# Performance work log

Measured on AMD Instinct MI355X. Metric: run time of the kernel, lower is better.

The kernel has to match this reference:

```python
import jax, jax.numpy as jnp
import numpy as np

BN_EPS = 1e-5

def setup_inputs() -> dict:
    key = jax.random.key(0)
    k1, k2, k3 = jax.random.split(key, 3)
    B, N, K, C, Cout = 8, 16384, 16, 128, 256
    x = jax.random.normal(k1, (B, N, C), dtype=jnp.float32)
    edge_index = jax.random.randint(k2, (B, N, K), 0, N, dtype=jnp.int64)
    W = jax.random.normal(k3, (Cout, 2 * C), dtype=jnp.float32) * (1.0 / np.sqrt(2 * C))
    b = jnp.zeros((Cout,), dtype=jnp.float32)
    gamma = jnp.ones((Cout,), dtype=jnp.float32)
    beta = jnp.zeros((Cout,), dtype=jnp.float32)
    return {"x": x, "edge_index": edge_index, "W": W, "b": b, "gamma": gamma, "beta": beta}

def reference(x, edge_index, W, b, gamma, beta):
    B, N, C = x.shape
    # gather neighbors: [B, N, K, C]
    neighbors = x[jnp.arange(B)[:, None, None], edge_index]
    # max-relative aggregation: max_j x_j - x_i
    agg = neighbors.max(axis=2) - x                      # [B, N, C]
    h = jnp.concatenate([x, agg], axis=-1).reshape(B * N, 2 * C)
    y = h @ W.T + b                                      # Linear -> [B*N, Cout]
    # BatchNorm1d (training mode: batch statistics, biased variance)
    mean = y.mean(axis=0)
    var = y.var(axis=0)
    y = (y - mean) * jax.lax.rsqrt(var + BN_EPS) * gamma + beta
    out = jax.nn.gelu(y, approximate=False)
    return out.reshape(B, N, -1)
```

## Files before the change

### kernel.cpp

```cpp
#include <hip/hip_runtime.h>
#include <math.h>

constexpr int B_ = 8;
constexpr int N_ = 16384;
constexpr int C_ = 128;
constexpr int K_ = 16;
constexpr int CO = 256;
constexpr int TC = 256;
constexpr int M_ = B_ * N_;
constexpr int TM = 64;
constexpr int NB = M_ / TM;
constexpr int NCHUNK = 8;

typedef _Float16 h8 __attribute__((ext_vector_type(8)));
typedef float f4 __attribute__((ext_vector_type(4)));

__device__ __forceinline__ float4 f4max(float4 a, float4 b) {
  return make_float4(fmaxf(a.x, b.x), fmaxf(a.y, b.y),
                     fmaxf(a.z, b.z), fmaxf(a.w, b.w));
}

__device__ __forceinline__ ushort4 pack_h4(float4 v) {
  union { _Float16 h[4]; ushort4 u; } cv;
  cv.h[0] = (_Float16)v.x; cv.h[1] = (_Float16)v.y;
  cv.h[2] = (_Float16)v.z; cv.h[3] = (_Float16)v.w;
  return cv.u;
}

__global__ void k0_prep(const float* __restrict__ W, _Float16* __restrict__ Wf) {
  int g = blockIdx.x * 256 + threadIdx.x;
  int cout = g >> 5;
  int G = g & 31;
  int kk = G >> 2, go = G & 3;
  int nt = cout >> 4, c15 = cout & 15;
  const float* src = W + (size_t)cout * TC + G * 8;
  _Float16* dst = Wf + kk * 8192 + nt * 512 + (c15 + 16 * go) * 8;
  #pragma unroll
  for (int j = 0; j < 8; ++j) dst[j] = (_Float16)src[j];
}

__global__ __launch_bounds__(256, 3)
void k1_fused(const float* __restrict__ x, const int* __restrict__ eidx,
              const _Float16* __restrict__ Wf, const float* __restrict__ bias,
              float* __restrict__ y, double* __restrict__ stats)
{
  __shared__ __align__(16) _Float16 hsf[TM * TC];
  __shared__ __align__(16) int ids[TM * K_];

  const int tid = threadIdx.x;
  const int wave = tid >> 6;
  const int lane = tid & 63;
  const int batch = blockIdx.x & 7;
  const int tile = blockIdx.x >> 3;
  const long long row0 = (long long)batch * N_ + (long long)tile * TM;
  const float* __restrict__ xb = x + (size_t)batch * N_ * C_;

  ((int4*)ids)[tid] = ((const int4*)(eidx + row0 * K_))[tid];
  __syncthreads();

  #pragma unroll
  for (int it = 0; it < 8; ++it) {
    int w = it * 256 + tid;
    int m = w >> 5;
    int cq = (w & 31) << 2;
    float4 xv = *(const float4*)(x + (row0 + m) * (size_t)C_ + cq);
    float4 mx = make_float4(-INFINITY, -INFINITY, -INFINITY, -INFINITY);
    #pragma unroll
    for (int j = 0; j < K_; ++j) {
      int nb = ids[m * K_ + j];
      mx = f4max(mx, *(const float4*)(xb + (size_t)nb * C_ + cq));
    }
    int a0 = ((m >> 4) << 13) | ((cq >> 3) << 8) | ((m & 15) << 4) | ((cq & 4) << 1);
    a0 ^= ((a0 >> 8) & 7) << 4;
    *(ushort4*)((char*)hsf + a0) = pack_h4(xv);
    float4 dv = make_float4(mx.x - xv.x, mx.y - xv.y, mx.z - xv.z, mx.w - xv.w);
    int c2 = 128 + cq;
    int a1 = ((m >> 4) << 13) | ((c2 >> 3) << 8) | ((m & 15) << 4) | ((c2 & 4) << 1);
    a1 ^= ((a1 >> 8) & 7) << 4;
    *(ushort4*)((char*)hsf + a1) = pack_h4(dv);
  }
  __syncthreads();

  f4 acc[4][4] = {};
  #pragma unroll
  for (int kk = 0; kk < NCHUNK; ++kk) {
    h8 af[4], bf[4];
    #pragma unroll
    for (int nt = 0; nt < 4; ++nt)
      bf[nt] = *(const h8*)((const char*)Wf + (kk << 14) + (wave << 12) + (nt << 10) + (lane << 4));
    #pragma unroll
    for (int mt = 0; mt < 4; ++mt) {
      int off = (mt << 13) + (kk << 10) + lane * 16;
      off ^= ((off >> 8) & 7) << 4;
      af[mt] = *(const h8*)((const char*)hsf + off);
    }
    #pragma unroll
    for (int mt = 0; mt < 4; ++mt)
      #pragma unroll
      for (int nt = 0; nt < 4; ++nt)
        acc[mt][nt] = __builtin_amdgcn_mfma_f32_16x16x32_f16(af[mt], bf[nt], acc[mt][nt], 0, 0, 0);
  }

  const int c15 = lane & 15;
  const int rg = lane >> 4;
  float s4[4] = {0.f, 0.f, 0.f, 0.f};
  float q4[4] = {0.f, 0.f, 0.f, 0.f};
  #pragma unroll
  for (int nt = 0; nt < 4; ++nt) {
    int col = (wave << 6) + (nt << 4) + c15;
    float bb = bias[col];
    #pragma unroll
    for (int mt = 0; mt < 4; ++mt) {
      #pragma unroll
      for (int r = 0; r < 4; ++r) {
        float v = acc[mt][nt][r] + bb;
        long long row = row0 + (mt << 4) + (rg << 2) + r;
        y[row * CO + col] = v;
        s4[nt] += v;
        q4[nt] += v * v;
      }
    }
  }
  #pragma unroll
  for (int nt = 0; nt < 4; ++nt) {
    s4[nt] += __shfl_xor(s4[nt], 16, 64);
    s4[nt] += __shfl_xor(s4[nt], 32, 64);
    q4[nt] += __shfl_xor(q4[nt], 16, 64);
    q4[nt] += __shfl_xor(q4[nt], 32, 64);
  }
  if (lane < 16) {
    #pragma unroll
    for (int nt = 0; nt < 4; ++nt) {
      int col = (wave << 6) + (nt << 4) + c15;
      atomicAdd(&stats[col], (double)s4[nt]);
      atomicAdd(&stats[col + 256], (double)q4[nt]);
    }
  }
}

__global__ void k2_stats(const double* __restrict__ stats,
                         const float* __restrict__ gamma,
                         const float* __restrict__ beta,
                         float* __restrict__ ss) {
  int c = threadIdx.x;
  double mean = stats[c] * (1.0 / M_);
  double var  = stats[256 + c] * (1.0 / M_) - mean * mean;
  double scale = (double)gamma[c] / sqrt(var + 1e-5);
  ss[c]       = (float)scale;
  ss[256 + c] = (float)((double)beta[c] - mean * scale);
}

__global__ __launch_bounds__(256)
void k3_bn_gelu(float* __restrict__ y, const float* __restrict__ ss) {
  __shared__ float s_sc[CO], s_sh[CO];
  s_sc[threadIdx.x] = ss[threadIdx.x];
  s_sh[threadIdx.x] = ss[256 + threadIdx.x];
  __syncthreads();
  const float inv_sqrt2 = 0.70710678118654752440f;
  size_t i = (size_t)blockIdx.x * blockDim.x + threadIdx.x;
  const size_t stride = (size_t)gridDim.x * blockDim.x;
  const size_t total = (size_t)M_ * CO / 4;
  float4* y4 = (float4*)y;
  for (; i < total; i += stride) {
    float4 v = y4[i];
    int c4 = (int)(i & (CO / 4 - 1)) * 4;
    float4 r;
    { float u = v.x * s_sc[c4 + 0] + s_sh[c4 + 0]; r.x = 0.5f * u * (1.f + erff(u * inv_sqrt2)); }
    { float u = v.y * s_sc[c4 + 1] + s_sh[c4 + 1]; r.y = 0.5f * u * (1.f + erff(u * inv_sqrt2)); }
    { float u = v.z * s_sc[c4 + 2] + s_sh[c4 + 2]; r.z = 0.5f * u * (1.f + erff(u * inv_sqrt2)); }
    { float u = v.w * s_sc[c4 + 3] + s_sh[c4 + 3]; r.w = 0.5f * u * (1.f + erff(u * inv_sqrt2)); }
    y4[i] = r;
  }
}

extern "C" void kernel_launch(void* const* d_in, const int* in_sizes, int n_in,
                              void* d_out, int out_size, void* d_ws, size_t ws_size,
                              hipStream_t stream)
{
  const float* x     = (const float*)d_in[0];
  const int*   eidx  = (const int*)d_in[1];
  const float* W     = (const float*)d_in[2];
  const float* bias  = (const float*)d_in[3];
  const float* gamma = (const float*)d_in[4];
  const float* beta  = (const float*)d_in[5];
  float* y = (float*)d_out;
  char* ws = (char*)d_ws;

  _Float16* Wf    = (_Float16*)ws;
  double*   stats = (double*)(ws + 131072);
  float*    ss    = (float*)(ws + 131072 + 4096);

  hipMemsetAsync(stats, 0, 512 * sizeof(double), stream);
  k0_prep<<<32, 256, 0, stream>>>(W, Wf);
  k1_fused<<<NB, 256, 0, stream>>>(x, eidx, Wf, bias, y, stats);
  k2_stats<<<1, 256, 0, stream>>>(stats, gamma, beta, ss);
  k3_bn_gelu<<<2048, 256, 0, stream>>>(y, ss);
}
```

Measured before the change: 324.8 us.

## Gather neighbors from fp16 copy of x and use polynomial erf in GELU

Adds a pre-pass that converts x to fp16 in workspace, so the neighbor gather and max in the fused kernel read half the bytes and work on 8 channels per load. The fp32 path is kept as a fallback when the workspace is too small. The BN+GELU kernel replaces erff with an Abramowitz-Stegun polynomial approximation and loads scale/shift once per thread into registers instead of shared memory. Occupancy hint on the fused kernel rises from 3 to 4. This adds an extra conversion pass over x and some precision loss in the gather, max and GELU.

```diff
diff --git a/kernel.cpp b/kernel.cpp
--- a/kernel.cpp
+++ b/kernel.cpp
@@ -27,6 +27,32 @@
   return cv.u;
 }
 
+__device__ __forceinline__ uint4 hmax4(uint4 a, uint4 b) {
+  union U { uint4 u; _Float16 h[8]; } ua, ub, r;
+  ua.u = a; ub.u = b;
+  #pragma unroll
+  for (int i = 0; i < 8; ++i) r.h[i] = ua.h[i] > ub.h[i] ? ua.h[i] : ub.h[i];
+  return r.u;
+}
+
+__device__ __forceinline__ uint4 hsub4(uint4 a, uint4 b) {
+  union U { uint4 u; _Float16 h[8]; } ua, ub, r;
+  ua.u = a; ub.u = b;
+  #pragma unroll
+  for (int i = 0; i < 8; ++i) r.h[i] = ua.h[i] - ub.h[i];
+  return r.u;
+}
+
+__device__ __forceinline__ float gelu_f(float u) {
+  float z = fabsf(u) * 0.70710678118654752f;
+  float t = 1.0f / (1.0f + 0.3275911f * z);
+  float p = t * (0.254829592f + t * (-0.284496736f + t * (1.421413741f +
+            t * (-1.453152027f + t * 1.061405429f))));
+  float erfz = 1.0f - p * __expf(-z * z);
+  erfz = copysignf(erfz, u);
+  return 0.5f * u * (1.0f + erfz);
+}
+
 __global__ void k0_prep(const float* __restrict__ W, _Float16* __restrict__ Wf) {
   int g = blockIdx.x * 256 + threadIdx.x;
   int cout = g >> 5;
@@ -39,10 +65,22 @@
   for (int j = 0; j < 8; ++j) dst[j] = (_Float16)src[j];
 }
 
-__global__ __launch_bounds__(256, 3)
+__global__ __launch_bounds__(256)
+void k0b_cvt(const float* __restrict__ x, _Float16* __restrict__ xh) {
+  const size_t total = (size_t)M_ * C_ / 4;
+  const size_t stride = (size_t)gridDim.x * 256;
+  for (size_t i = (size_t)blockIdx.x * 256 + threadIdx.x; i < total; i += stride) {
+    float4 a = ((const float4*)x)[i];
+    ((ushort4*)xh)[i] = pack_h4(a);
+  }
+}
+
+template <int FP16>
+__global__ __launch_bounds__(256, 4)
 void k1_fused(const float* __restrict__ x, const int* __restrict__ eidx,
               const _Float16* __restrict__ Wf, const float* __restrict__ bias,
-              float* __restrict__ y, double* __restrict__ stats)
+              float* __restrict__ y, double* __restrict__ stats,
+              const _Float16* __restrict__ xh)
 {
   __shared__ __align__(16) _Float16 hsf[TM * TC];
   __shared__ __align__(16) int ids[TM * K_];
@@ -53,31 +91,56 @@
   const int batch = blockIdx.x & 7;
   const int tile = blockIdx.x >> 3;
   const long long row0 = (long long)batch * N_ + (long long)tile * TM;
-  const float* __restrict__ xb = x + (size_t)batch * N_ * C_;
 
   ((int4*)ids)[tid] = ((const int4*)(eidx + row0 * K_))[tid];
   __syncthreads();
 
-  #pragma unroll
-  for (int it = 0; it < 8; ++it) {
-    int w = it * 256 + tid;
-    int m = w >> 5;
-    int cq = (w & 31) << 2;
-    float4 xv = *(const float4*)(x + (row0 + m) * (size_t)C_ + cq);
-    float4 mx = make_float4(-INFINITY, -INFINITY, -INFINITY, -INFINITY);
-    #pragma unroll
-    for (int j = 0; j < K_; ++j) {
-      int nb = ids[m * K_ + j];
-      mx = f4max(mx, *(const float4*)(xb + (size_t)nb * C_ + cq));
-    }
-    int a0 = ((m >> 4) << 13) | ((cq >> 3) << 8) | ((m & 15) << 4) | ((cq & 4) << 1);
-    a0 ^= ((a0 >> 8) & 7) << 4;
-    *(ushort4*)((char*)hsf + a0) = pack_h4(xv);
-    float4 dv = make_float4(mx.x - xv.x, mx.y - xv.y, mx.z - xv.z, mx.w - xv.w);
-    int c2 = 128 + cq;
-    int a1 = ((m >> 4) << 13) | ((c2 >> 3) << 8) | ((m & 15) << 4) | ((c2 & 4) << 1);
-    a1 ^= ((a1 >> 8) & 7) << 4;
-    *(ushort4*)((char*)hsf + a1) = pack_h4(dv);
+  if constexpr (FP16) {
+    const _Float16* __restrict__ xbh = xh + (size_t)batch * N_ * C_;
+    #pragma unroll
+    for (int it = 0; it < 4; ++it) {
+      int w = it * 256 + tid;
+      int m = w >> 4;
+      int ch8 = (w & 15) << 3;
+      uint4 xv = *(const uint4*)(xh + (row0 + m) * (size_t)C_ + ch8);
+      uint4 mx = *(const uint4*)(xbh + (size_t)ids[m * K_] * C_ + ch8);
+      #pragma unroll
+      for (int j = 1; j < K_; ++j) {
+        int nb = ids[m * K_ + j];
+        mx = hmax4(mx, *(const uint4*)(xbh + (size_t)nb * C_ + ch8));
+      }
+      uint4 dv = hsub4(mx, xv);
+      int a0 = ((m >> 4) << 13) | ((ch8 >> 3) << 8) | ((m & 15) << 4);
+      a0 ^= ((a0 >> 8) & 7) << 4;
+      *(uint4*)((char*)hsf + a0) = xv;
+      int c2 = 128 + ch8;
+      int a1 = ((m >> 4) << 13) | ((c2 >> 3) << 8) | ((m & 15) << 4);
+      a1 ^= ((a1 >> 8) & 7) << 4;
+      *(uint4*)((char*)hsf + a1) = dv;
+    }
+  } else {
+    const float* __restrict__ xb = x + (size_t)batch * N_ * C_;
+    #pragma unroll
+    for (int it = 0; it < 8; ++it) {
+      int w = it * 256 + tid;
+      int m = w >> 5;
+      int cq = (w & 31) << 2;
+      float4 xv = *(const float4*)(x + (row0 + m) * (size_t)C_ + cq);
+      float4 mx = make_float4(-INFINITY, -INFINITY, -INFINITY, -INFINITY);
+      #pragma unroll
+      for (int j = 0; j < K_; ++j) {
+        int nb = ids[m * K_ + j];
+        mx = f4max(mx, *(const float4*)(xb + (size_t)nb * C_ + cq));
+      }
+      int a0 = ((m >> 4) << 13) | ((cq >> 3) << 8) | ((m & 15) << 4) | ((cq & 4) << 1);
+      a0 ^= ((a0 >> 8) & 7) << 4;
+      *(ushort4*)((char*)hsf + a0) = pack_h4(xv);
+      float4 dv = make_float4(mx.x - xv.x, mx.y - xv.y, mx.z - xv.z, mx.w - xv.w);
+      int c2 = 128 + cq;
+      int a1 = ((m >> 4) << 13) | ((c2 >> 3) << 8) | ((m & 15) << 4) | ((cq & 4) << 1);
+      a1 ^= ((a1 >> 8) & 7) << 4;
+      *(ushort4*)((char*)hsf + a1) = pack_h4(dv);
+    }
   }
   __syncthreads();
 
@@ -152,23 +215,20 @@
 
 __global__ __launch_bounds__(256)
 void k3_bn_gelu(float* __restrict__ y, const float* __restrict__ ss) {
-  __shared__ float s_sc[CO], s_sh[CO];
-  s_sc[threadIdx.x] = ss[threadIdx.x];
-  s_sh[threadIdx.x] = ss[256 + threadIdx.x];
-  __syncthreads();
-  const float inv_sqrt2 = 0.70710678118654752440f;
   size_t i = (size_t)blockIdx.x * blockDim.x + threadIdx.x;
   const size_t stride = (size_t)gridDim.x * blockDim.x;
   const size_t total = (size_t)M_ * CO / 4;
+  int c4 = (int)(i & (CO / 4 - 1)) * 4;
+  float4 sc = *(const float4*)(ss + c4);
+  float4 sh = *(const float4*)(ss + 256 + c4);
   float4* y4 = (float4*)y;
   for (; i < total; i += stride) {
     float4 v = y4[i];
-    int c4 = (int)(i & (CO / 4 - 1)) * 4;
     float4 r;
-    { float u = v.x * s_sc[c4 + 0] + s_sh[c4 + 0]; r.x = 0.5f * u * (1.f + erff(u * inv_sqrt2)); }
-    { float u = v.y * s_sc[c4 + 1] + s_sh[c4 + 1]; r.y = 0.5f * u * (1.f + erff(u * inv_sqrt2)); }
-    { float u = v.z * s_sc[c4 + 2] + s_sh[c4 + 2]; r.z = 0.5f * u * (1.f + erff(u * inv_sqrt2)); }
-    { float u = v.w * s_sc[c4 + 3] + s_sh[c4 + 3]; r.w = 0.5f * u * (1.f + erff(u * inv_sqrt2)); }
+    r.x = gelu_f(v.x * sc.x + sh.x);
+    r.y = gelu_f(v.y * sc.y + sh.y);
+    r.z = gelu_f(v.z * sc.z + sh.z);
+    r.w = gelu_f(v.w * sc.w + sh.w);
     y4[i] = r;
   }
 }
@@ -189,10 +249,18 @@
   _Float16* Wf    = (_Float16*)ws;
   double*   stats = (double*)(ws + 131072);
   float*    ss    = (float*)(ws + 131072 + 4096);
-
-  hipMemsetAsync(stats, 0, 512 * sizeof(double), stream);
+  _Float16* xh    = (_Float16*)(ws + (1 << 20));
+  const size_t ws_needed = (1 << 20) + (size_t)M_ * C_ * 2;
+  const bool fp16path = ws_size >= ws_needed;
+
+  (void)hipMemsetAsync(stats, 0, 512 * sizeof(double), stream);
   k0_prep<<<32, 256, 0, stream>>>(W, Wf);
-  k1_fused<<<NB, 256, 0, stream>>>(x, eidx, Wf, bias, y, stats);
+  if (fp16path) {
+    k0b_cvt<<<2048, 256, 0, stream>>>(x, xh);
+    k1_fused<1><<<NB, 256, 0, stream>>>(x, eidx, Wf, bias, y, stats, xh);
+  } else {
+    k1_fused<0><<<NB, 256, 0, stream>>>(x, eidx, Wf, bias, y, stats, nullptr);
+  }
   k2_stats<<<1, 256, 0, stream>>>(stats, gamma, beta, ss);
   k3_bn_gelu<<<2048, 256, 0, stream>>>(y, ss);
 }
```

Result: faster. 296.6 us (-8.7%).
